# Performance work log

Measured on AMD Instinct MI355X. Metric: run time of the kernel, lower is better.

The kernel has to match this reference:

```python
import jax, jax.numpy as jnp
import numpy as np

N_NODES = 50000
N_EDGES = 800000


def gcn_conv(x, edge_index, W, b, n_nodes):
    """PyG GCNConv: h = x @ W; add self-loops; symmetric D^-1/2 A D^-1/2 aggregation; + bias."""
    h = x @ W  # [N, out]
    loops = jnp.arange(n_nodes, dtype=edge_index.dtype)
    row = jnp.concatenate([edge_index[0], loops])  # source nodes
    col = jnp.concatenate([edge_index[1], loops])  # target nodes
    deg = jax.ops.segment_sum(jnp.ones_like(col, dtype=h.dtype), col, num_segments=n_nodes)
    deg_inv_sqrt = jnp.where(deg > 0, jax.lax.rsqrt(deg), 0.0)
    norm = deg_inv_sqrt[row] * deg_inv_sqrt[col]  # [E+N]
    msg = h[row] * norm[:, None]  # gather + scale
    out = jax.ops.segment_sum(msg, col, num_segments=n_nodes)  # scatter-add
    return out + b


def setup_inputs() -> dict:
    key = jax.random.key(0)
    k_x, k_ei, k_w1, k_w2 = jax.random.split(key, 4)
    x = jax.random.normal(k_x, (N_NODES, 9), dtype=jnp.float32)
    edge_index = jax.random.randint(k_ei, (2, N_EDGES), 0, N_NODES, dtype=jnp.int64)
    # Glorot-like init for the linear weights
    W1 = jax.random.normal(k_w1, (9, 100), dtype=jnp.float32) * (1.0 / np.sqrt(9.0))
    b1 = jnp.zeros((100,), dtype=jnp.float32)
    W2 = jax.random.normal(k_w2, (100, 1), dtype=jnp.float32) * (1.0 / np.sqrt(100.0))
    b2 = jnp.zeros((1,), dtype=jnp.float32)
    return {"x": x, "edge_index": edge_index, "W1": W1, "b1": b1, "W2": W2, "b2": b2}


def reference(x, edge_index, W1, b1, W2, b2):
    n = x.shape[0]
    h = jax.nn.relu(gcn_conv(x, edge_index, W1, b1, n))
    return gcn_conv(h, edge_index, W2, b2, n)  # [N, 1]
```

## Files before the change

### kernel.cpp

```cpp
#include <hip/hip_runtime.h>

#define N_NODES 50000
#define N_EDGES 800000
#define FIN 9
#define FH 100
#define XS_W 12
#define NP 256
#define NPB 196
#define PCAP 3584
#define EPB 2048

__global__ __launch_bounds__(256) void k_partition(const int* __restrict__ row,
                                                   const int* __restrict__ col,
                                                   int* __restrict__ gpcnt,
                                                   int* __restrict__ part_ebuf, int e) {
    __shared__ int histA[NP];
    __shared__ int scanA[NP];
    __shared__ int baseA[NP];
    __shared__ int curA[NP];
    __shared__ int stage[EPB];
    int t = threadIdx.x;
    int e0 = blockIdx.x * EPB;
    int nE = min(EPB, e - e0);
    histA[t] = 0;
    __syncthreads();

    int epack[EPB / 256];
    int cntl = 0;
    for (int i = t; i < nE; i += 256) {
        int r = row[e0 + i], c = col[e0 + i];
        int p = c / NPB;
        int ln = c - p * NPB;
        epack[cntl++] = (r << 16) | (p << 8) | ln;
        atomicAdd(&histA[p], 1);
    }
    __syncthreads();
    scanA[t] = histA[t];
    __syncthreads();
    for (int off = 1; off < NP; off <<= 1) {
        int tmp = (t >= off) ? scanA[t - off] : 0;
        __syncthreads();
        scanA[t] += tmp;
        __syncthreads();
    }
    scanA[t] -= histA[t];
    curA[t] = scanA[t];
    baseA[t] = atomicAdd(&gpcnt[t], histA[t]);
    __syncthreads();
    for (int i = 0; i < cntl; ++i) {
        unsigned u = (unsigned)epack[i];
        int p = (u >> 8) & 255;
        int L = atomicAdd(&curA[p], 1);
        stage[L] = epack[i];
    }
    __syncthreads();
    for (int s = t; s < nE; s += 256) {
        int v = stage[s];
        int p = ((unsigned)v >> 8) & 255;
        int idx = baseA[p] + (s - scanA[p]);
        if (idx < PCAP) part_ebuf[p * PCAP + idx] = v;
    }
}

__global__ __launch_bounds__(512) void k_csr_build(const int* __restrict__ gpcnt,
                                                   const int* __restrict__ part_ebuf,
                                                   const float* __restrict__ x,
                                                   int* __restrict__ csr,
                                                   int* __restrict__ start,
                                                   int* __restrict__ cnt,
                                                   float* __restrict__ xs, int n) {
    __shared__ int histB[NP];
    __shared__ int scanB[NP];
    __shared__ int curB[NP];
    __shared__ int stageR[PCAP];
    int t = threadIdx.x;
    int p = blockIdx.x;
    int m = min(gpcnt[p], PCAP);
    if (t < NP) histB[t] = 0;
    __syncthreads();

    int epack[(PCAP + 511) / 512];
    int cntl = 0;
    for (int j = t; j < m; j += 512) {
        int v = part_ebuf[p * PCAP + j];
        epack[cntl++] = v;
        atomicAdd(&histB[((unsigned)v) & 255], 1);
    }
    __syncthreads();
    if (t < NP) scanB[t] = histB[t];
    __syncthreads();
    for (int off = 1; off < NP; off <<= 1) {
        int tmp = (t < NP && t >= off) ? scanB[t - off] : 0;
        __syncthreads();
        if (t < NP) scanB[t] += tmp;
        __syncthreads();
    }
    if (t < NP) {
        scanB[t] -= histB[t];
        curB[t] = scanB[t];
    }
    __syncthreads();
    for (int i = 0; i < cntl; ++i) {
        unsigned u = (unsigned)epack[i];
        int L = atomicAdd(&curB[u & 255], 1);
        stageR[L] = (int)(u >> 16);
    }
    __syncthreads();
    for (int s = t; s < m; s += 512) csr[p * PCAP + s] = stageR[s];

    int ln = t;
    int v = p * NPB + ln;
    if (ln < NPB && v < n) {
        int d = histB[ln];
        start[v] = p * PCAP + scanB[ln];
        cnt[v] = d;
        float dv = rsqrtf((float)(d + 1));
        float* xr = &xs[(size_t)v * XS_W];
#pragma unroll
        for (int k = 0; k < FIN; ++k) xr[k] = dv * x[v * FIN + k];
        xr[9] = dv; xr[10] = 0.0f; xr[11] = 0.0f;
    }
}

__global__ __launch_bounds__(256) void k_gather_dense4(const float4* __restrict__ xs4,
                                                       const int* __restrict__ csr,
                                                       const int* __restrict__ start,
                                                       const int* __restrict__ cnt,
                                                       const float* __restrict__ W1,
                                                       const float* __restrict__ b1,
                                                       const float* __restrict__ W2,
                                                       float* __restrict__ ps, int n) {
    __shared__ float sW1[FIN * FH];
    __shared__ float sb1[FH];
    __shared__ float sW2[FH];
    int t = threadIdx.x;
    for (int i = t; i < FIN * FH; i += 256) sW1[i] = W1[i];
    for (int i = t; i < FH; i += 256) { sb1[i] = b1[i]; sW2[i] = W2[i]; }
    __syncthreads();

    int idx = blockIdx.x * 256 + t;
    int v = idx >> 2;
    int l4 = t & 3;
    if (v >= n) return;

    float4 a0 = make_float4(0, 0, 0, 0), a1 = a0;
    float a8 = 0.0f;
    int s = start[v], m = cnt[v];
    for (int j = l4; j < m; j += 4) {
        int r = csr[s + j];
        float4 q0 = xs4[r * 3], q1 = xs4[r * 3 + 1], q2 = xs4[r * 3 + 2];
        a0.x += q0.x; a0.y += q0.y; a0.z += q0.z; a0.w += q0.w;
        a1.x += q1.x; a1.y += q1.y; a1.z += q1.z; a1.w += q1.w;
        a8 += q2.x;
    }
#pragma unroll
    for (int off = 1; off < 4; off <<= 1) {
        a0.x += __shfl_xor(a0.x, off); a0.y += __shfl_xor(a0.y, off);
        a0.z += __shfl_xor(a0.z, off); a0.w += __shfl_xor(a0.w, off);
        a1.x += __shfl_xor(a1.x, off); a1.y += __shfl_xor(a1.y, off);
        a1.z += __shfl_xor(a1.z, off); a1.w += __shfl_xor(a1.w, off);
        a8   += __shfl_xor(a8, off);
    }
    float4 s0 = xs4[v * 3], s1 = xs4[v * 3 + 1], s2 = xs4[v * 3 + 2];
    float dv = s2.y;
    float xa[FIN];
    xa[0] = dv * (a0.x + s0.x); xa[1] = dv * (a0.y + s0.y);
    xa[2] = dv * (a0.z + s0.z); xa[3] = dv * (a0.w + s0.w);
    xa[4] = dv * (a1.x + s1.x); xa[5] = dv * (a1.y + s1.y);
    xa[6] = dv * (a1.z + s1.z); xa[7] = dv * (a1.w + s1.w);
    xa[8] = dv * (a8 + s2.x);

    float pv = 0.0f;
    for (int j = l4; j < FH; j += 4) {
        float h = sb1[j];
#pragma unroll
        for (int k = 0; k < FIN; ++k) h = fmaf(xa[k], sW1[k * FH + j], h);
        h = fmaxf(h, 0.0f);
        pv = fmaf(h, sW2[j], pv);
    }
    pv += __shfl_xor(pv, 1);
    pv += __shfl_xor(pv, 2);
    if (l4 == 0) ps[v] = dv * pv;
}

__global__ __launch_bounds__(256) void k_out4(const int* __restrict__ csr,
                                              const int* __restrict__ start,
                                              const int* __restrict__ cnt,
                                              const float* __restrict__ ps,
                                              const float* __restrict__ xs,
                                              const float* __restrict__ b2,
                                              float* __restrict__ out, int n) {
    int t = threadIdx.x;
    int idx = blockIdx.x * 256 + t;
    int v = idx >> 2;
    int l4 = t & 3;
    if (v >= n) return;
    int s = start[v], m = cnt[v];
    float sum = 0.0f;
    for (int j = l4; j < m; j += 4) sum += ps[csr[s + j]];
    sum += __shfl_xor(sum, 1);
    sum += __shfl_xor(sum, 2);
    if (l4 == 0) {
        float dv = xs[(size_t)v * XS_W + 9];
        out[v] = dv * (sum + ps[v]) + b2[0];
    }
}

__global__ void k_count(const int* __restrict__ col, int* __restrict__ ideg, int e) {
    int i = blockIdx.x * blockDim.x + threadIdx.x;
    if (i < e) atomicAdd(&ideg[col[i]], 1);
}
__global__ void k_offsets(const int* __restrict__ ideg, int* __restrict__ start,
                          int* __restrict__ cursor, float* __restrict__ dinv,
                          int* __restrict__ counter, int n) {
    __shared__ int sdata[256];
    __shared__ int sbase;
    int t = threadIdx.x;
    int v = blockIdx.x * 256 + t;
    int d = (v < n) ? ideg[v] : 0;
    sdata[t] = d;
    __syncthreads();
    for (int off = 1; off < 256; off <<= 1) {
        int tmp = (t >= off) ? sdata[t - off] : 0;
        __syncthreads();
        sdata[t] += tmp;
        __syncthreads();
    }
    if (t == 255) sbase = atomicAdd(counter, sdata[255]);
    __syncthreads();
    if (v < n) {
        int excl = sdata[t] - d;
        start[v] = sbase + excl;
        cursor[v] = sbase + excl;
        dinv[v] = rsqrtf((float)(d + 1));
    }
}
__global__ void k_bucket(const int* __restrict__ row, const int* __restrict__ col,
                         int* __restrict__ cursor, int* __restrict__ csr, int e) {
    int i = blockIdx.x * blockDim.x + threadIdx.x;
    if (i >= e) return;
    int pos = atomicAdd(&cursor[col[i]], 1);
    csr[pos] = row[i];
}
__global__ void k_gather_dense(const float* __restrict__ x, const int* __restrict__ csr,
                               const int* __restrict__ start, const int* __restrict__ ideg,
                               const float* __restrict__ dinv, const float* __restrict__ W1,
                               const float* __restrict__ b1, const float* __restrict__ W2,
                               float* __restrict__ p, int n) {
    __shared__ float sW1[FIN * FH];
    __shared__ float sb1[FH];
    __shared__ float sW2[FH];
    int t = threadIdx.x;
    for (int i = t; i < FIN * FH; i += blockDim.x) sW1[i] = W1[i];
    for (int i = t; i < FH; i += blockDim.x) { sb1[i] = b1[i]; sW2[i] = W2[i]; }
    __syncthreads();
    int v = blockIdx.x * blockDim.x + t;
    if (v >= n) return;
    float acc[FIN];
#pragma unroll
    for (int k = 0; k < FIN; ++k) acc[k] = 0.0f;
    int s = start[v], cntv = ideg[v];
    for (int j = 0; j < cntv; ++j) {
        int r = csr[s + j];
        float w = dinv[r];
#pragma unroll
        for (int k = 0; k < FIN; ++k) acc[k] = fmaf(w, x[r * FIN + k], acc[k]);
    }
    float dvv = dinv[v];
    float self = dvv * dvv;
    float xa[FIN];
#pragma unroll
    for (int k = 0; k < FIN; ++k) xa[k] = acc[k] * dvv + x[v * FIN + k] * self;
    float pv = 0.0f;
    for (int j = 0; j < FH; ++j) {
        float h = sb1[j];
#pragma unroll
        for (int k = 0; k < FIN; ++k) h = fmaf(xa[k], sW1[k * FH + j], h);
        h = fmaxf(h, 0.0f);
        pv = fmaf(h, sW2[j], pv);
    }
    p[v] = pv;
}
__global__ void k_out(const int* __restrict__ csr, const int* __restrict__ start,
                      const int* __restrict__ ideg, const float* __restrict__ dinv,
                      const float* __restrict__ p, const float* __restrict__ b2,
                      float* __restrict__ out, int n) {
    int v = blockIdx.x * blockDim.x + threadIdx.x;
    if (v >= n) return;
    int s = start[v], cntv = ideg[v];
    float sum = 0.0f;
    for (int j = 0; j < cntv; ++j) sum = fmaf(dinv[csr[s + j]], p[csr[s + j]], sum);
    float dvv = dinv[v];
    out[v] = dvv * sum + p[v] * dvv * dvv + b2[0];
}

extern "C" void kernel_launch(void* const* d_in, const int* in_sizes, int n_in,
                              void* d_out, int out_size, void* d_ws, size_t ws_size,
                              hipStream_t stream) {
    const float* x  = (const float*)d_in[0];
    const int*   ei = (const int*)d_in[1];
    const float* W1 = (const float*)d_in[2];
    const float* b1 = (const float*)d_in[3];
    const float* W2 = (const float*)d_in[4];
    const float* b2 = (const float*)d_in[5];
    float* out = (float*)d_out;

    const int n = N_NODES;
    const int e = N_EDGES;
    const int* row = ei;
    const int* col = ei + e;

    const int B = 256;
    int gn = (n + B - 1) / B;
    int gn4 = (4 * n + B - 1) / B;
    int ge = (e + B - 1) / B;

    size_t need = ((size_t)n * XS_W + 2u * NP * PCAP + NP + 3u * n) * sizeof(int);
    if (ws_size >= need) {
        float* xs      = (float*)d_ws;
        int* part_ebuf = (int*)(xs + (size_t)n * XS_W);
        int* csr       = part_ebuf + (size_t)NP * PCAP;
        int* gpcnt     = csr + (size_t)NP * PCAP;
        int* startA    = gpcnt + NP;
        int* cntA      = startA + n;
        float* ps      = (float*)(cntA + n);

        hipMemsetAsync(gpcnt, 0, NP * sizeof(int), stream);
        int ga = (e + EPB - 1) / EPB;
        k_partition<<<ga, B, 0, stream>>>(row, col, gpcnt, part_ebuf, e);
        k_csr_build<<<NP, 512, 0, stream>>>(gpcnt, part_ebuf, x, csr, startA, cntA, xs, n);
        k_gather_dense4<<<gn4, B, 0, stream>>>((const float4*)xs, csr, startA, cntA,
                                               W1, b1, W2, ps, n);
        k_out4<<<gn4, B, 0, stream>>>(csr, startA, cntA, ps, xs, b2, out, n);
    } else {
        int* ideg    = (int*)d_ws;
        int* counter = ideg + n;
        int* startA  = counter + 1;
        int* cursor  = startA + n;
        float* dinv  = (float*)(cursor + n);
        float* p     = dinv + n;
        int* csr     = (int*)(p + n);

        hipMemsetAsync(ideg, 0, (size_t)(n + 1) * sizeof(int), stream);
        k_count<<<ge, B, 0, stream>>>(col, ideg, e);
        k_offsets<<<gn, B, 0, stream>>>(ideg, startA, cursor, dinv, counter, n);
        k_bucket<<<ge, B, 0, stream>>>(row, col, cursor, csr, e);
        k_gather_dense<<<gn, B, 0, stream>>>(x, csr, startA, ideg, dinv, W1, b1, W2, p, n);
        k_out<<<gn, B, 0, stream>>>(csr, startA, ideg, dinv, p, b2, out, n);
    }
}
```

Measured before the change: 57.60 us.

## Fuse four GCN stages into one persistent kernel with software grid barriers

Replaces the partition, CSR build, layer-1 gather/dense and layer-2 output kernels with a single persistent kernel of 512 blocks that loops over work and synchronises through atomic-counter grid barriers. The aim is to remove three kernel launch gaps and their tail drain between dependent stages. In exchange it relies on all 512 blocks being co-resident (launch_bounds 256,2), which risks deadlock if occupancy is insufficient. It also lowers the CSR-build stage from 512 to 256 threads per partition and spends spin time at each barrier.

```diff
diff --git a/kernel.cpp b/kernel.cpp
--- a/kernel.cpp
+++ b/kernel.cpp
@@ -9,200 +9,210 @@
 #define NPB 196
 #define PCAP 3584
 #define EPB 2048
-
-__global__ __launch_bounds__(256) void k_partition(const int* __restrict__ row,
-                                                   const int* __restrict__ col,
-                                                   int* __restrict__ gpcnt,
-                                                   int* __restrict__ part_ebuf, int e) {
-    __shared__ int histA[NP];
-    __shared__ int scanA[NP];
-    __shared__ int baseA[NP];
-    __shared__ int curA[NP];
-    __shared__ int stage[EPB];
+#define GRID_C 512
+
+__device__ __forceinline__ void grid_barrier(int* ctr, int nb) {
+    __syncthreads();
+    if (threadIdx.x == 0) {
+        __threadfence();
+        if (atomicAdd(ctr, 1) + 1 < nb) {
+            while (__hip_atomic_load(ctr, __ATOMIC_RELAXED, __HIP_MEMORY_SCOPE_AGENT) < nb)
+                __builtin_amdgcn_s_sleep(2);
+        }
+        __threadfence();
+    }
+    __syncthreads();
+}
+
+__global__ __launch_bounds__(256, 2) void k_mega(
+        const int* __restrict__ row, const int* __restrict__ col,
+        const float* __restrict__ x, const float* __restrict__ W1,
+        const float* __restrict__ b1, const float* __restrict__ W2,
+        const float* __restrict__ b2,
+        int* __restrict__ gpcnt, int* __restrict__ bar,
+        int* __restrict__ part_ebuf, int* __restrict__ csr,
+        int* __restrict__ startA, int* __restrict__ cntA,
+        float* __restrict__ xs, float* __restrict__ ps,
+        float* __restrict__ out, int n, int e) {
+    __shared__ int smem[3 * NP + PCAP];
     int t = threadIdx.x;
-    int e0 = blockIdx.x * EPB;
-    int nE = min(EPB, e - e0);
-    histA[t] = 0;
-    __syncthreads();
-
-    int epack[EPB / 256];
-    int cntl = 0;
-    for (int i = t; i < nE; i += 256) {
-        int r = row[e0 + i], c = col[e0 + i];
-        int p = c / NPB;
-        int ln = c - p * NPB;
-        epack[cntl++] = (r << 16) | (p << 8) | ln;
-        atomicAdd(&histA[p], 1);
-    }
-    __syncthreads();
-    scanA[t] = histA[t];
-    __syncthreads();
-    for (int off = 1; off < NP; off <<= 1) {
-        int tmp = (t >= off) ? scanA[t - off] : 0;
+    int nb = gridDim.x;
+
+    {
+        int* hist = smem;
+        int* scan = smem + NP;
+        int* base = smem + 2 * NP;
+        int* cur  = smem + 3 * NP;
+        int* stage = smem + 4 * NP;
+        int nchunks = (e + EPB - 1) / EPB;
+        for (int chunk = blockIdx.x; chunk < nchunks; chunk += nb) {
+            int e0 = chunk * EPB;
+            int nE = min(EPB, e - e0);
+            hist[t] = 0;
+            __syncthreads();
+            int epack[EPB / 256];
+            int cntl = 0;
+            for (int i = t; i < nE; i += 256) {
+                int r = row[e0 + i], c = col[e0 + i];
+                int p = c / NPB;
+                int ln = c - p * NPB;
+                epack[cntl++] = (r << 16) | (p << 8) | ln;
+                atomicAdd(&hist[p], 1);
+            }
+            __syncthreads();
+            scan[t] = hist[t];
+            __syncthreads();
+            for (int off = 1; off < NP; off <<= 1) {
+                int tmp = (t >= off) ? scan[t - off] : 0;
+                __syncthreads();
+                scan[t] += tmp;
+                __syncthreads();
+            }
+            scan[t] -= hist[t];
+            cur[t] = scan[t];
+            base[t] = atomicAdd(&gpcnt[t], hist[t]);
+            __syncthreads();
+            for (int i = 0; i < cntl; ++i) {
+                unsigned u = (unsigned)epack[i];
+                int p = (u >> 8) & 255;
+                int L = atomicAdd(&cur[p], 1);
+                stage[L] = (int)u;
+            }
+            __syncthreads();
+            for (int s2 = t; s2 < nE; s2 += 256) {
+                int v = stage[s2];
+                int p = ((unsigned)v >> 8) & 255;
+                int idx = base[p] + (s2 - scan[p]);
+                if (idx < PCAP) part_ebuf[p * PCAP + idx] = v;
+            }
+            __syncthreads();
+        }
+    }
+    grid_barrier(&bar[0], nb);
+
+    {
+        int* hist = smem;
+        int* scan = smem + NP;
+        int* cur  = smem + 2 * NP;
+        int* stageR = smem + 3 * NP;
+        for (int p = blockIdx.x; p < NP; p += nb) {
+            int m = min(gpcnt[p], PCAP);
+            hist[t] = 0;
+            __syncthreads();
+            int epack[(PCAP + 255) / 256];
+            int cntl = 0;
+            for (int j = t; j < m; j += 256) {
+                int v = part_ebuf[p * PCAP + j];
+                epack[cntl++] = v;
+                atomicAdd(&hist[((unsigned)v) & 255], 1);
+            }
+            __syncthreads();
+            scan[t] = hist[t];
+            __syncthreads();
+            for (int off = 1; off < NP; off <<= 1) {
+                int tmp = (t >= off) ? scan[t - off] : 0;
+                __syncthreads();
+                scan[t] += tmp;
+                __syncthreads();
+            }
+            scan[t] -= hist[t];
+            cur[t] = scan[t];
+            __syncthreads();
+            for (int i = 0; i < cntl; ++i) {
+                unsigned u = (unsigned)epack[i];
+                int L = atomicAdd(&cur[u & 255], 1);
+                stageR[L] = (int)(u >> 16);
+            }
+            __syncthreads();
+            for (int s2 = t; s2 < m; s2 += 256) csr[p * PCAP + s2] = stageR[s2];
+
+            int ln = t;
+            int v = p * NPB + ln;
+            if (ln < NPB && v < n) {
+                int d = hist[ln];
+                startA[v] = p * PCAP + scan[ln];
+                cntA[v] = d;
+                float dv = rsqrtf((float)(d + 1));
+                float* xr = &xs[(size_t)v * XS_W];
+#pragma unroll
+                for (int k = 0; k < FIN; ++k) xr[k] = dv * x[v * FIN + k];
+                xr[9] = dv; xr[10] = 0.0f; xr[11] = 0.0f;
+            }
+            __syncthreads();
+        }
+    }
+    grid_barrier(&bar[1], nb);
+
+    {
+        float* sW1 = (float*)smem;
+        float* sb1 = sW1 + FIN * FH;
+        float* sW2 = sb1 + FH;
+        for (int i = t; i < FIN * FH; i += 256) sW1[i] = W1[i];
+        for (int i = t; i < FH; i += 256) { sb1[i] = b1[i]; sW2[i] = W2[i]; }
         __syncthreads();
-        scanA[t] += tmp;
-        __syncthreads();
-    }
-    scanA[t] -= histA[t];
-    curA[t] = scanA[t];
-    baseA[t] = atomicAdd(&gpcnt[t], histA[t]);
-    __syncthreads();
-    for (int i = 0; i < cntl; ++i) {
-        unsigned u = (unsigned)epack[i];
-        int p = (u >> 8) & 255;
-        int L = atomicAdd(&curA[p], 1);
-        stage[L] = epack[i];
-    }
-    __syncthreads();
-    for (int s = t; s < nE; s += 256) {
-        int v = stage[s];
-        int p = ((unsigned)v >> 8) & 255;
-        int idx = baseA[p] + (s - scanA[p]);
-        if (idx < PCAP) part_ebuf[p * PCAP + idx] = v;
-    }
-}
-
-__global__ __launch_bounds__(512) void k_csr_build(const int* __restrict__ gpcnt,
-                                                   const int* __restrict__ part_ebuf,
-                                                   const float* __restrict__ x,
-                                                   int* __restrict__ csr,
-                                                   int* __restrict__ start,
-                                                   int* __restrict__ cnt,
-                                                   float* __restrict__ xs, int n) {
-    __shared__ int histB[NP];
-    __shared__ int scanB[NP];
-    __shared__ int curB[NP];
-    __shared__ int stageR[PCAP];
-    int t = threadIdx.x;
-    int p = blockIdx.x;
-    int m = min(gpcnt[p], PCAP);
-    if (t < NP) histB[t] = 0;
-    __syncthreads();
-
-    int epack[(PCAP + 511) / 512];
-    int cntl = 0;
-    for (int j = t; j < m; j += 512) {
-        int v = part_ebuf[p * PCAP + j];
-        epack[cntl++] = v;
-        atomicAdd(&histB[((unsigned)v) & 255], 1);
-    }
-    __syncthreads();
-    if (t < NP) scanB[t] = histB[t];
-    __syncthreads();
-    for (int off = 1; off < NP; off <<= 1) {
-        int tmp = (t < NP && t >= off) ? scanB[t - off] : 0;
-        __syncthreads();
-        if (t < NP) scanB[t] += tmp;
-        __syncthreads();
-    }
-    if (t < NP) {
-        scanB[t] -= histB[t];
-        curB[t] = scanB[t];
-    }
-    __syncthreads();
-    for (int i = 0; i < cntl; ++i) {
-        unsigned u = (unsigned)epack[i];
-        int L = atomicAdd(&curB[u & 255], 1);
-        stageR[L] = (int)(u >> 16);
-    }
-    __syncthreads();
-    for (int s = t; s < m; s += 512) csr[p * PCAP + s] = stageR[s];
-
-    int ln = t;
-    int v = p * NPB + ln;
-    if (ln < NPB && v < n) {
-        int d = histB[ln];
-        start[v] = p * PCAP + scanB[ln];
-        cnt[v] = d;
-        float dv = rsqrtf((float)(d + 1));
-        float* xr = &xs[(size_t)v * XS_W];
-#pragma unroll
-        for (int k = 0; k < FIN; ++k) xr[k] = dv * x[v * FIN + k];
-        xr[9] = dv; xr[10] = 0.0f; xr[11] = 0.0f;
-    }
-}
-
-__global__ __launch_bounds__(256) void k_gather_dense4(const float4* __restrict__ xs4,
-                                                       const int* __restrict__ csr,
-                                                       const int* __restrict__ start,
-                                                       const int* __restrict__ cnt,
-                                                       const float* __restrict__ W1,
-                                                       const float* __restrict__ b1,
-                                                       const float* __restrict__ W2,
-                                                       float* __restrict__ ps, int n) {
-    __shared__ float sW1[FIN * FH];
-    __shared__ float sb1[FH];
-    __shared__ float sW2[FH];
-    int t = threadIdx.x;
-    for (int i = t; i < FIN * FH; i += 256) sW1[i] = W1[i];
-    for (int i = t; i < FH; i += 256) { sb1[i] = b1[i]; sW2[i] = W2[i]; }
-    __syncthreads();
-
-    int idx = blockIdx.x * 256 + t;
-    int v = idx >> 2;
-    int l4 = t & 3;
-    if (v >= n) return;
-
-    float4 a0 = make_float4(0, 0, 0, 0), a1 = a0;
-    float a8 = 0.0f;
-    int s = start[v], m = cnt[v];
-    for (int j = l4; j < m; j += 4) {
-        int r = csr[s + j];
-        float4 q0 = xs4[r * 3], q1 = xs4[r * 3 + 1], q2 = xs4[r * 3 + 2];
-        a0.x += q0.x; a0.y += q0.y; a0.z += q0.z; a0.w += q0.w;
-        a1.x += q1.x; a1.y += q1.y; a1.z += q1.z; a1.w += q1.w;
-        a8 += q2.x;
-    }
-#pragma unroll
-    for (int off = 1; off < 4; off <<= 1) {
-        a0.x += __shfl_xor(a0.x, off); a0.y += __shfl_xor(a0.y, off);
-        a0.z += __shfl_xor(a0.z, off); a0.w += __shfl_xor(a0.w, off);
-        a1.x += __shfl_xor(a1.x, off); a1.y += __shfl_xor(a1.y, off);
-        a1.z += __shfl_xor(a1.z, off); a1.w += __shfl_xor(a1.w, off);
-        a8   += __shfl_xor(a8, off);
-    }
-    float4 s0 = xs4[v * 3], s1 = xs4[v * 3 + 1], s2 = xs4[v * 3 + 2];
-    float dv = s2.y;
-    float xa[FIN];
-    xa[0] = dv * (a0.x + s0.x); xa[1] = dv * (a0.y + s0.y);
-    xa[2] = dv * (a0.z + s0.z); xa[3] = dv * (a0.w + s0.w);
-    xa[4] = dv * (a1.x + s1.x); xa[5] = dv * (a1.y + s1.y);
-    xa[6] = dv * (a1.z + s1.z); xa[7] = dv * (a1.w + s1.w);
-    xa[8] = dv * (a8 + s2.x);
-
-    float pv = 0.0f;
-    for (int j = l4; j < FH; j += 4) {
-        float h = sb1[j];
-#pragma unroll
-        for (int k = 0; k < FIN; ++k) h = fmaf(xa[k], sW1[k * FH + j], h);
-        h = fmaxf(h, 0.0f);
-        pv = fmaf(h, sW2[j], pv);
-    }
-    pv += __shfl_xor(pv, 1);
-    pv += __shfl_xor(pv, 2);
-    if (l4 == 0) ps[v] = dv * pv;
-}
-
-__global__ __launch_bounds__(256) void k_out4(const int* __restrict__ csr,
-                                              const int* __restrict__ start,
-                                              const int* __restrict__ cnt,
-                                              const float* __restrict__ ps,
-                                              const float* __restrict__ xs,
-                                              const float* __restrict__ b2,
-                                              float* __restrict__ out, int n) {
-    int t = threadIdx.x;
-    int idx = blockIdx.x * 256 + t;
-    int v = idx >> 2;
-    int l4 = t & 3;
-    if (v >= n) return;
-    int s = start[v], m = cnt[v];
-    float sum = 0.0f;
-    for (int j = l4; j < m; j += 4) sum += ps[csr[s + j]];
-    sum += __shfl_xor(sum, 1);
-    sum += __shfl_xor(sum, 2);
-    if (l4 == 0) {
-        float dv = xs[(size_t)v * XS_W + 9];
-        out[v] = dv * (sum + ps[v]) + b2[0];
+        const float4* xs4 = (const float4*)xs;
+        int total = 4 * n;
+        for (int idx = blockIdx.x * 256 + t; idx < total; idx += nb * 256) {
+            int v = idx >> 2;
+            int l4 = idx & 3;
+            float4 a0 = make_float4(0, 0, 0, 0), a1 = a0;
+            float a8 = 0.0f;
+            int s = startA[v], m = cntA[v];
+            for (int j = l4; j < m; j += 4) {
+                int r = csr[s + j];
+                float4 q0 = xs4[r * 3], q1 = xs4[r * 3 + 1], q2 = xs4[r * 3 + 2];
+                a0.x += q0.x; a0.y += q0.y; a0.z += q0.z; a0.w += q0.w;
+                a1.x += q1.x; a1.y += q1.y; a1.z += q1.z; a1.w += q1.w;
+                a8 += q2.x;
+            }
+#pragma unroll
+            for (int off = 1; off < 4; off <<= 1) {
+                a0.x += __shfl_xor(a0.x, off); a0.y += __shfl_xor(a0.y, off);
+                a0.z += __shfl_xor(a0.z, off); a0.w += __shfl_xor(a0.w, off);
+                a1.x += __shfl_xor(a1.x, off); a1.y += __shfl_xor(a1.y, off);
+                a1.z += __shfl_xor(a1.z, off); a1.w += __shfl_xor(a1.w, off);
+                a8   += __shfl_xor(a8, off);
+            }
+            float4 s0 = xs4[v * 3], s1 = xs4[v * 3 + 1], s2 = xs4[v * 3 + 2];
+            float dv = s2.y;
+            float xa[FIN];
+            xa[0] = dv * (a0.x + s0.x); xa[1] = dv * (a0.y + s0.y);
+            xa[2] = dv * (a0.z + s0.z); xa[3] = dv * (a0.w + s0.w);
+            xa[4] = dv * (a1.x + s1.x); xa[5] = dv * (a1.y + s1.y);
+            xa[6] = dv * (a1.z + s1.z); xa[7] = dv * (a1.w + s1.w);
+            xa[8] = dv * (a8 + s2.x);
+
+            float pv = 0.0f;
+            for (int j = l4; j < FH; j += 4) {
+                float h = sb1[j];
+#pragma unroll
+                for (int k = 0; k < FIN; ++k) h = fmaf(xa[k], sW1[k * FH + j], h);
+                h = fmaxf(h, 0.0f);
+                pv = fmaf(h, sW2[j], pv);
+            }
+            pv += __shfl_xor(pv, 1);
+            pv += __shfl_xor(pv, 2);
+            if (l4 == 0) ps[v] = dv * pv;
+        }
+    }
+    grid_barrier(&bar[2], nb);
+
+    {
+        int total = 4 * n;
+        float bias = b2[0];
+        for (int idx = blockIdx.x * 256 + t; idx < total; idx += nb * 256) {
+            int v = idx >> 2;
+            int l4 = idx & 3;
+            int s = startA[v], m = cntA[v];
+            float sum = 0.0f;
+            for (int j = l4; j < m; j += 4) sum += ps[csr[s + j]];
+            sum += __shfl_xor(sum, 1);
+            sum += __shfl_xor(sum, 2);
+            if (l4 == 0) {
+                float dv = xs[(size_t)v * XS_W + 9];
+                out[v] = dv * (sum + ps[v]) + bias;
+            }
+        }
     }
 }
 
@@ -312,26 +322,23 @@
 
     const int B = 256;
     int gn = (n + B - 1) / B;
-    int gn4 = (4 * n + B - 1) / B;
     int ge = (e + B - 1) / B;
 
-    size_t need = ((size_t)n * XS_W + 2u * NP * PCAP + NP + 3u * n) * sizeof(int);
+    size_t need = ((size_t)n * (XS_W + 3) + NP + 8 + 2u * NP * PCAP) * sizeof(int);
     if (ws_size >= need) {
         float* xs      = (float*)d_ws;
-        int* part_ebuf = (int*)(xs + (size_t)n * XS_W);
-        int* csr       = part_ebuf + (size_t)NP * PCAP;
-        int* gpcnt     = csr + (size_t)NP * PCAP;
-        int* startA    = gpcnt + NP;
+        int* gpcnt     = (int*)(xs + (size_t)n * XS_W);
+        int* bar       = gpcnt + NP;
+        int* startA    = bar + 8;
         int* cntA      = startA + n;
         float* ps      = (float*)(cntA + n);
-
-        hipMemsetAsync(gpcnt, 0, NP * sizeof(int), stream);
-        int ga = (e + EPB - 1) / EPB;
-        k_partition<<<ga, B, 0, stream>>>(row, col, gpcnt, part_ebuf, e);
-        k_csr_build<<<NP, 512, 0, stream>>>(gpcnt, part_ebuf, x, csr, startA, cntA, xs, n);
-        k_gather_dense4<<<gn4, B, 0, stream>>>((const float4*)xs, csr, startA, cntA,
-                                               W1, b1, W2, ps, n);
-        k_out4<<<gn4, B, 0, stream>>>(csr, startA, cntA, ps, xs, b2, out, n);
+        int* part_ebuf = (int*)(ps + n);
+        int* csr       = part_ebuf + (size_t)NP * PCAP;
+
+        hipMemsetAsync(gpcnt, 0, (NP + 8) * sizeof(int), stream);
+        k_mega<<<GRID_C, B, 0, stream>>>(row, col, x, W1, b1, W2, b2,
+                                         gpcnt, bar, part_ebuf, csr,
+                                         startA, cntA, xs, ps, out, n, e);
     } else {
         int* ideg    = (int*)d_ws;
         int* counter = ideg + n;
```

Measured after the change: 192.5 us. 234% more time.
